# Kernel optimization log

Measured on AMD Instinct MI355X. Metric: run time of the kernel, lower is better.

The kernel has to match this reference:

```python
import jax, jax.numpy as jnp
import numpy as np

EPS = 1e-5        # BatchNorm eps (torch default)
ALPHA = 0.2       # LeakyReLU negative slope


def _gather_nbrs(x, idx):
    # x: (B,N,C), idx: (B,P,S) -> (B,P,S,C)
    B, P, S = idx.shape
    flat = jnp.take_along_axis(x, idx.reshape(B, P * S, 1), axis=1)
    return flat.reshape(B, P, S, x.shape[-1])


def _mlp_layer(x, w, b, g, bt, m, v):
    # 1x1 Conv2d == channel matmul; BN in eval mode with running stats; ReLU.
    h = x @ w.T + b
    h = (h - m) * jax.lax.rsqrt(v + EPS) * g + bt
    return jax.nn.relu(h)


def setup_inputs() -> dict:
    key = jax.random.key(0)
    ks = jax.random.split(key, 8)
    B, N, P, S, C = 16, 4096, 1024, 32, 64
    inp = {
        "xyz": jax.random.normal(ks[0], (B, 3, N), dtype=jnp.float32),
        "points": jax.random.normal(ks[1], (B, C, N), dtype=jnp.float32),
        "fps_idx": jax.random.randint(ks[2], (B, P), 0, N, dtype=jnp.int32),
        "group_idx": jax.random.randint(ks[3], (B, P, S), 0, N, dtype=jnp.int32),
    }
    chans = [(64, 67), (64, 64), (128, 64)]
    for i, (co, ci) in enumerate(chans, start=1):
        kk = jax.random.fold_in(key, 100 + i)
        inp[f"w{i}"] = jax.random.normal(kk, (co, ci), dtype=jnp.float32) * (1.0 / np.sqrt(ci))
        inp[f"b{i}"] = jnp.zeros((co,), jnp.float32)
        inp[f"g{i}"] = jnp.ones((co,), jnp.float32)
        inp[f"beta{i}"] = jnp.zeros((co,), jnp.float32)
        inp[f"m{i}"] = jnp.zeros((co,), jnp.float32)
        inp[f"v{i}"] = jnp.ones((co,), jnp.float32)
    inp["a"] = jax.random.normal(ks[4], (3 + 128, 128), dtype=jnp.float32) * 0.1
    return inp


def reference(xyz, points, fps_idx, group_idx,
              w1, b1, g1, beta1, m1, v1,
              w2, b2, g2, beta2, m2, v2,
              w3, b3, g3, beta3, m3, v3, a):
    xyz_p = jnp.transpose(xyz, (0, 2, 1))      # (B,N,3)
    pts_p = jnp.transpose(points, (0, 2, 1))   # (B,N,C)

    # sample_and_group with precomputed fps / ball-query indices
    new_xyz = jnp.take_along_axis(xyz_p, fps_idx[:, :, None], axis=1)   # (B,P,3)
    fps_feat = jnp.take_along_axis(pts_p, fps_idx[:, :, None], axis=1)  # (B,P,C)
    grouped_xyz = _gather_nbrs(xyz_p, group_idx) - new_xyz[:, :, None, :]  # relative (B,P,S,3)
    grouped_feat = _gather_nbrs(pts_p, group_idx)                           # (B,P,S,C)

    new_points = jnp.concatenate([grouped_xyz, grouped_feat], axis=-1)  # (B,P,S,3+C)
    fps_points = jnp.concatenate([new_xyz, fps_feat], axis=-1)          # (B,P,3+C)

    layers = [(w1, b1, g1, beta1, m1, v1), (w2, b2, g2, beta2, m2, v2), (w3, b3, g3, beta3, m3, v3)]
    for (w, b, g, bt, m, v) in layers:
        new_points = _mlp_layer(new_points, w, b, g, bt, m, v)
        fps_points = _mlp_layer(fps_points, w, b, g, bt, m, v)

    # GraphAttention: delta features -> leaky-relu scores -> softmax over neighbors -> pool
    delta_p = new_xyz[:, :, None, :] - grouped_xyz        # (B,P,S,3)
    delta_h = fps_points[:, :, None, :] - new_points       # (B,P,S,D)
    e = jnp.concatenate([delta_p, delta_h], axis=-1) @ a   # (B,P,S,D)
    e = jnp.where(e > 0, e, ALPHA * e)
    attn = jax.nn.softmax(e, axis=2)                       # softmax over nsample
    pooled = jnp.sum(attn * new_points, axis=2)            # (B,P,D)

    return jnp.transpose(new_xyz, (0, 2, 1)), jnp.transpose(pooled, (0, 2, 1))
```

## Files before the change

kernel.cpp:

```cpp
#include <hip/hip_runtime.h>
#include <hip/hip_bf16.h>

#define Bn 16
#define Nn 4096
#define Pn 1024
#define Sn 32
#define Cn 64
#define EPSn 1e-5f
#define ALPHAn 0.2f
#define LOG2E 1.44269504088896341f

#define W1O 0
#define W2O 4352
#define W3O 8448
#define AO  16640
#define B1O 33536
#define B2O 33600
#define B3O 33664
#define WSF 33792
__device__ __align__(16) float g_W[WSF];

#define F1F 0
#define F2F 24
#define F3F 40
#define F5F 72
#define NFRAG 152
#define WFU (NFRAG * 512)
__device__ __align__(16) unsigned short g_Wf[WFU];

__device__ __align__(16) float g_pts[Bn * Nn * 68];
__device__ __align__(16) float g_fps[Bn * Pn * 132];
__device__ __align__(16) float g_tmp[Bn * Pn * 128];

typedef __attribute__((ext_vector_type(8))) short short8;
typedef __attribute__((ext_vector_type(4))) float f32x4;

__device__ __forceinline__ void split2(float v, unsigned short& hu, unsigned short& lu) {
  __hip_bfloat16 h = __float2bfloat16(v);
  float hv = __bfloat162float(h);
  __hip_bfloat16 l = __float2bfloat16(v - hv);
  hu = *(unsigned short*)&h;
  lu = *(unsigned short*)&l;
}
__device__ __forceinline__ unsigned short bfh(float v) {
  __hip_bfloat16 h = __float2bfloat16(v);
  return *(unsigned short*)&h;
}

#define MFMA_BF16 __builtin_amdgcn_mfma_f32_16x16x32_bf16
#define TERM3(Ci, Ahh, All, Bh, Bl) \
    Ci = MFMA_BF16(Ahh, Bh, Ci, 0, 0, 0); \
    Ci = MFMA_BF16(Ahh, Bl, Ci, 0, 0, 0); \
    Ci = MFMA_BF16(All, Bh, Ci, 0, 0, 0);

#define ST_PK(BUF, ST, ROW, COLE, V) do {                                   \
    float _pp = __shfl_xor((V), 1);                                         \
    unsigned _pk;                                                           \
    asm("v_cvt_pk_bf16_f32 %0, %1, %2" : "=v"(_pk) : "v"(V), "v"(_pp));     \
    if (!(nn & 1)) *(unsigned*)((BUF) + (ROW) * (ST) + (COLE)) = _pk;       \
  } while (0)

__global__ __launch_bounds__(256) void prep_kernel(
    const float* __restrict__ xyz, const float* __restrict__ points,
    const float* __restrict__ w1, const float* __restrict__ b1,
    const float* __restrict__ g1, const float* __restrict__ bt1,
    const float* __restrict__ m1, const float* __restrict__ v1,
    const float* __restrict__ w2, const float* __restrict__ b2,
    const float* __restrict__ g2, const float* __restrict__ bt2,
    const float* __restrict__ m2, const float* __restrict__ v2,
    const float* __restrict__ w3, const float* __restrict__ b3,
    const float* __restrict__ g3, const float* __restrict__ bt3,
    const float* __restrict__ m3, const float* __restrict__ v3,
    const float* __restrict__ a)
{
  if (blockIdx.x < 1024) {
    __shared__ float T[68 * 65];
    const int t = threadIdx.x;
    const int b = blockIdx.x >> 6, n0 = (blockIdx.x & 63) << 6;
    const int nn = t & 63, cgrp = t >> 6;
    #pragma unroll
    for (int k = 0; k < 16; ++k) {
      const int c = cgrp * 16 + k;
      T[c * 65 + nn] = points[(b * Cn + c) * Nn + n0 + nn];
    }
    if (cgrp == 0) {
      #pragma unroll
      for (int d = 0; d < 3; ++d)
        T[(64 + d) * 65 + nn] = xyz[(b * 3 + d) * Nn + n0 + nn];
      T[67 * 65 + nn] = 0.f;
    }
    __syncthreads();
    const int row = t >> 2, part = t & 3;
    float* dst = g_pts + (((long)b << 12) + n0 + row) * 68 + part * 16;
    #pragma unroll
    for (int j = 0; j < 4; ++j) {
      const int o = part * 16 + j * 4;
      float4 v = { T[(o + 0) * 65 + row], T[(o + 1) * 65 + row],
                   T[(o + 2) * 65 + row], T[(o + 3) * 65 + row] };
      *(float4*)(dst + j * 4) = v;
    }
    if (part == 3) {
      float4 v = { T[64 * 65 + row], T[65 * 65 + row],
                   T[66 * 65 + row], T[67 * 65 + row] };
      *(float4*)(dst + 16) = v;
    }
    return;
  }
  const int idx = (blockIdx.x - 1024) * blockDim.x + threadIdx.x;
  if (idx < WSF) {
    float val;
    if (idx < W2O) {
      const int k = idx >> 6, o = idx & 63;
      const float sc = g1[o] * rsqrtf(v1[o] + EPSn);
      val = (k < 64) ? w1[o * 67 + 3 + k] * sc
          : (k < 67) ? w1[o * 67 + (k - 64)] * sc : 0.f;
    } else if (idx < W3O) {
      const int r = idx - W2O, k = r >> 6, o = r & 63;
      val = w2[o * 64 + k] * (g2[o] * rsqrtf(v2[o] + EPSn));
    } else if (idx < AO) {
      const int r = idx - W3O, k = r >> 7, o = r & 127;
      val = w3[o * 64 + k] * (g3[o] * rsqrtf(v3[o] + EPSn));
    } else if (idx < B1O) {
      int r = idx - AO;
      const int half = r / 8448; r -= half * 8448;
      const int k = r >> 6, o = half * 64 + (r & 63);
      val = (k < 128) ? a[(3 + k) * 128 + o]
          : (k < 131) ? a[(k - 128) * 128 + o] : 0.f;
    } else if (idx < B2O) {
      const int o = idx - B1O;
      val = (b1[o] - m1[o]) * (g1[o] * rsqrtf(v1[o] + EPSn)) + bt1[o];
    } else if (idx < B3O) {
      const int o = idx - B2O;
      val = (b2[o] - m2[o]) * (g2[o] * rsqrtf(v2[o] + EPSn)) + bt2[o];
    } else {
      const int o = idx - B3O;
      val = (b3[o] - m3[o]) * (g3[o] * rsqrtf(v3[o] + EPSn)) + bt3[o];
    }
    g_W[idx] = val;
  } else if (idx < WSF + WFU) {
    const int i = idx - WSF;
    const int frag = i >> 9, r = i & 511;
    const int lane = r >> 3, j = r & 7;
    const int quad = lane >> 4, nn = lane & 15;
    int plane, n, k;
    float w;
    if (frag < F2F) {
      const int f = frag;
      plane = f & 1;
      const int c = (f >> 1) & 1, kcch = f >> 2, kc = kcch % 3, ch = kcch / 3;
      n = ch * 32 + c * 16 + nn; k = kc * 32 + quad * 8 + j;
      const float s = g1[n] * rsqrtf(v1[n] + EPSn);
      w = (k < 64) ? w1[n * 67 + 3 + k] * s
        : (k < 67) ? w1[n * 67 + (k - 64)] * s : 0.f;
    } else if (frag < F3F) {
      const int f = frag - F2F;
      plane = f & 1;
      const int c = (f >> 1) & 1, kc = (f >> 2) & 1, ch = f >> 3;
      n = ch * 32 + c * 16 + nn; k = kc * 32 + quad * 8 + j;
      w = w2[n * 64 + k] * (g2[n] * rsqrtf(v2[n] + EPSn));
    } else if (frag < F5F) {
      const int f = frag - F3F;
      plane = f & 1;
      const int c = (f >> 1) & 3, kc = (f >> 3) & 1, ch = f >> 4;
      n = ch * 64 + c * 16 + nn; k = kc * 32 + quad * 8 + j;
      w = w3[n * 64 + k] * (g3[n] * rsqrtf(v3[n] + EPSn));
    } else {
      const int f = frag - F5F;
      plane = f & 1;
      const int c = (f >> 1) & 3, kcch = f >> 3, kc = kcch % 5, ch = kcch / 5;
      n = ch * 64 + c * 16 + nn; k = kc * 32 + quad * 8 + j;
      w = ((k < 128) ? a[(3 + k) * 128 + n]
        : (k < 131) ? a[(k - 128) * 128 + n] : 0.f) * LOG2E;
    }
    unsigned short hu, lu; split2(w, hu, lu);
    g_Wf[i] = plane ? lu : hu;
  }
}

#define XAs 88
#define XHs 152

__global__ __launch_bounds__(256) void fps_kernel(
    const int* __restrict__ fps_idx, float* __restrict__ out)
{
  __shared__ __align__(16) unsigned char LB[15376];
  unsigned short* XAh = (unsigned short*)(LB + 0);
  unsigned short* XAl = (unsigned short*)(LB + 2816);
  unsigned short* XHh = (unsigned short*)(LB + 5632);
  unsigned short* XHl = (unsigned short*)(LB + 10496);
  unsigned short* ZS  = (unsigned short*)(LB + 15360);

  const int t = threadIdx.x, lane = t & 63, w = t >> 6;
  const int quad = lane >> 4, nn = lane & 15;
  const int ch = w >> 1, cl = w & 1;
  const int blk = ((blockIdx.x & 7) << 7) | (blockIdx.x >> 3);
  const int g0 = blk * 16;

  if (t < 4) ((float*)ZS)[t] = 0.f;

  if (t < 128) {
    const int s0 = t >> 3, cg = t & 7;
    const int gp = g0 + s0, b = gp >> 10, p = gp & 1023;
    const int fi = fps_idx[gp];
    const float* frow = g_pts + (((long)b << 12) + fi) * 68;
    const int c0 = cg * 8;
    const float4 va = *(const float4*)(frow + c0);
    const float4 vb = *(const float4*)(frow + c0 + 4);
    short8 hv, lv;
    unsigned short hu, lu;
    split2(va.x, hu, lu); hv[0] = (short)hu; lv[0] = (short)lu;
    split2(va.y, hu, lu); hv[1] = (short)hu; lv[1] = (short)lu;
    split2(va.z, hu, lu); hv[2] = (short)hu; lv[2] = (short)lu;
    split2(va.w, hu, lu); hv[3] = (short)hu; lv[3] = (short)lu;
    split2(vb.x, hu, lu); hv[4] = (short)hu; lv[4] = (short)lu;
    split2(vb.y, hu, lu); hv[5] = (short)hu; lv[5] = (short)lu;
    split2(vb.z, hu, lu); hv[6] = (short)hu; lv[6] = (short)lu;
    split2(vb.w, hu, lu); hv[7] = (short)hu; lv[7] = (short)lu;
    *(short8*)(XAh + s0 * XAs + c0) = hv;
    *(short8*)(XAl + s0 * XAs + c0) = lv;
    if (cg == 0) {
      #pragma unroll
      for (int d = 0; d < 3; ++d) {
        const float v = frow[64 + d];
        unsigned short h2, l2; split2(v, h2, l2);
        XAh[s0 * XAs + 64 + d] = h2; XAl[s0 * XAs + 64 + d] = l2;
        XHh[s0 * XHs + 128 + d] = h2; XHl[s0 * XHs + 131 - 3 + d] = l2;
        XHl[s0 * XHs + 128 + d] = l2;
        out[(b * 3 + d) * Pn + p] = v;
        g_fps[(long)gp * 132 + 128 + d] = v;
      }
    } else if (cg == 1) {
      #pragma unroll
      for (int j = 0; j < 13; ++j) { XAh[s0 * XAs + 67 + j] = 0; XAl[s0 * XAs + 67 + j] = 0; }
    } else if (cg == 2) {
      #pragma unroll
      for (int j = 0; j < 13; ++j) { XHh[s0 * XHs + 131 + j] = 0; XHl[s0 * XHs + 131 + j] = 0; }
    }
  }
  __syncthreads();

  f32x4 C[2];
  const int col1 = w * 16 + nn;

  {
    const float bb = g_W[B1O + col1];
    C[0] = (f32x4){bb, bb, bb, bb};
  }
  #pragma unroll
  for (int kc = 0; kc < 3; ++kc) {
    const int ka = kc * 32 + quad * 8;
    const short8 A0h = (ka < 80) ? *(const short8*)(XAh + nn * XAs + ka) : *(const short8*)ZS;
    const short8 A0l = (ka < 80) ? *(const short8*)(XAl + nn * XAs + ka) : *(const short8*)ZS;
    const unsigned short* pf = g_Wf + (((ch * 3 + kc) * 2 + cl) * 2) * 512 + lane * 8;
    const short8 Bh = *(const short8*)pf, Bl = *(const short8*)(pf + 512);
    TERM3(C[0], A0h, A0l, Bh, Bl);
  }
  #pragma unroll
  for (int r = 0; r < 4; ++r) {
    const float v = fmaxf(C[0][r], 0.f);
    unsigned short hu, lu; split2(v, hu, lu);
    XHh[(quad * 4 + r) * XHs + col1] = hu;
    XHl[(quad * 4 + r) * XHs + col1] = lu;
  }
  __syncthreads();

  {
    const float bb = g_W[B2O + col1];
    C[0] = (f32x4){bb, bb, bb, bb};
  }
  #pragma unroll
  for (int kc = 0; kc < 2; ++kc) {
    const int ka = kc * 32 + quad * 8;
    const short8 A0h = *(const short8*)(XHh + nn * XHs + ka);
    const short8 A0l = *(const short8*)(XHl + nn * XHs + ka);
    const unsigned short* pf = g_Wf + (F2F + ((ch * 2 + kc) * 2 + cl) * 2) * 512 + lane * 8;
    const short8 Bh = *(const short8*)pf, Bl = *(const short8*)(pf + 512);
    TERM3(C[0], A0h, A0l, Bh, Bl);
  }
  __syncthreads();
  #pragma unroll
  for (int r = 0; r < 4; ++r) {
    const float v = fmaxf(C[0][r], 0.f);
    unsigned short hu, lu; split2(v, hu, lu);
    XAh[(quad * 4 + r) * XAs + col1] = hu;
    XAl[(quad * 4 + r) * XAs + col1] = lu;
  }
  __syncthreads();

  {
    const float b0 = g_W[B3O + w * 32 + nn];
    const float b1 = g_W[B3O + w * 32 + 16 + nn];
    C[0] = (f32x4){b0, b0, b0, b0};
    C[1] = (f32x4){b1, b1, b1, b1};
  }
  #pragma unroll
  for (int kc = 0; kc < 2; ++kc) {
    const int ka = kc * 32 + quad * 8;
    const short8 A0h = *(const short8*)(XAh + nn * XAs + ka);
    const short8 A0l = *(const short8*)(XAl + nn * XAs + ka);
    #pragma unroll
    for (int c2 = 0; c2 < 2; ++c2) {
      const unsigned short* pf = g_Wf + (F3F + ((ch * 2 + kc) * 4 + cl * 2 + c2) * 2) * 512 + lane * 8;
      const short8 Bh = *(const short8*)pf, Bl = *(const short8*)(pf + 512);
      TERM3(C[c2], A0h, A0l, Bh, Bl);
    }
  }
  __syncthreads();
  #pragma unroll
  for (int c2 = 0; c2 < 2; ++c2) {
    const int col = w * 32 + c2 * 16 + nn;
    #pragma unroll
    for (int r = 0; r < 4; ++r) {
      const float v = fmaxf(C[c2][r], 0.f);
      unsigned short hu, lu; split2(v, hu, lu);
      XHh[(quad * 4 + r) * XHs + col] = hu;
      XHl[(quad * 4 + r) * XHs + col] = lu;
    }
  }
  __syncthreads();

  C[0] = (f32x4){0.f,0.f,0.f,0.f}; C[1] = C[0];
  #pragma unroll
  for (int kc = 0; kc < 5; ++kc) {
    const int ka = kc * 32 + quad * 8;
    const short8 A0h = (ka < 144) ? *(const short8*)(XHh + nn * XHs + ka) : *(const short8*)ZS;
    const short8 A0l = (ka < 144) ? *(const short8*)(XHl + nn * XHs + ka) : *(const short8*)ZS;
    #pragma unroll
    for (int c2 = 0; c2 < 2; ++c2) {
      const unsigned short* pf = g_Wf + (F5F + ((ch * 5 + kc) * 4 + cl * 2 + c2) * 2) * 512 + lane * 8;
      const short8 Bh = *(const short8*)pf, Bl = *(const short8*)(pf + 512);
      TERM3(C[c2], A0h, A0l, Bh, Bl);
    }
  }
  #pragma unroll
  for (int c2 = 0; c2 < 2; ++c2) {
    const int col = w * 32 + c2 * 16 + nn;
    #pragma unroll
    for (int r = 0; r < 4; ++r)
      g_fps[(long)(g0 + quad * 4 + r) * 132 + col] = C[c2][r];
  }
}

__global__ __launch_bounds__(256) void transpose_out(float* __restrict__ out)
{
  __shared__ float T[64 * 129];
  const int t = threadIdx.x;
  const int b = blockIdx.x >> 4, p0 = (blockIdx.x & 15) << 6;
  const int c = t & 127, ph = t >> 7;
  #pragma unroll
  for (int pp = 0; pp < 32; ++pp) {
    const int pi = ph * 32 + pp;
    T[pi * 129 + c] = g_tmp[(((long)b << 10) + p0 + pi) * 128 + c];
  }
  __syncthreads();
  const int pn = t & 63, cg = t >> 6;
  #pragma unroll
  for (int k = 0; k < 32; ++k) {
    const int cc = cg * 32 + k;
    out[Bn * 3 * Pn + ((b << 7) + cc) * Pn + p0 + pn] = T[pn * 129 + cc];
  }
}

#define OXA 0
#define OXH 5632
#define OZS 15360
#define LDSB 15376

__global__ __launch_bounds__(256, 8) void fused_kernel(
    const int* __restrict__ group_idx)
{
  __shared__ __align__(16) unsigned char LB[LDSB];
  unsigned short* XAh = (unsigned short*)(LB + OXA);
  unsigned short* XHh = (unsigned short*)(LB + OXH);
  unsigned short* ZS  = (unsigned short*)(LB + OZS);

  const int t = threadIdx.x, lane = t & 63, w = t >> 6;
  const int quad = lane >> 4, nn = lane & 15;
  const int ch = w >> 1, cl = w & 1;
  const int g = ((blockIdx.x & 7) << 11) | (blockIdx.x >> 3);
  const int b = g >> 10;

  if (t < 4) ((float*)ZS)[t] = 0.f;

  {
    const int s0 = t >> 3, cg = t & 7;
    const int gi = group_idx[g * Sn + s0];
    const float* prow = g_pts + (((long)b << 12) + gi) * 68;
    const int c0 = cg * 8;
    const float4 va = *(const float4*)(prow + c0);
    const float4 vb = *(const float4*)(prow + c0 + 4);
    unsigned p0, p1, p2, p3;
    asm("v_cvt_pk_bf16_f32 %0, %1, %2" : "=v"(p0) : "v"(va.x), "v"(va.y));
    asm("v_cvt_pk_bf16_f32 %0, %1, %2" : "=v"(p1) : "v"(va.z), "v"(va.w));
    asm("v_cvt_pk_bf16_f32 %0, %1, %2" : "=v"(p2) : "v"(vb.x), "v"(vb.y));
    asm("v_cvt_pk_bf16_f32 %0, %1, %2" : "=v"(p3) : "v"(vb.z), "v"(vb.w));
    uint4 hv = {p0, p1, p2, p3};
    *(uint4*)(XAh + s0 * XAs + c0) = hv;
    if (cg == 0) {
      #pragma unroll
      for (int d = 0; d < 3; ++d) {
        const float r = prow[64 + d] - g_fps[(long)g * 132 + 128 + d];
        const unsigned short hu = bfh(r);
        XAh[s0 * XAs + 64 + d] = hu;
        XHh[s0 * XHs + 128 + d] = hu;
      }
    } else if (cg == 1) {
      #pragma unroll
      for (int j = 0; j < 13; ++j) XAh[s0 * XAs + 67 + j] = 0;
    } else if (cg == 2) {
      #pragma unroll
      for (int j = 0; j < 13; ++j) XHh[s0 * XHs + 131 + j] = 0;
    }
  }
  __syncthreads();

  f32x4 C[4];
  const int col1 = w * 16 + nn;
  const int colE1 = w * 16 + (nn & ~1);

  {
    const float bb = g_W[B1O + col1];
    C[0] = (f32x4){bb, bb, bb, bb};
    C[1] = C[0];
  }
  #pragma unroll
  for (int kc = 0; kc < 3; ++kc) {
    const int ka = kc * 32 + quad * 8;
    const short8 A0 = (ka < 80) ? *(const short8*)(XAh + nn * XAs + ka) : *(const short8*)ZS;
    const short8 A1 = (ka < 80) ? *(const short8*)(XAh + (16 + nn) * XAs + ka) : *(const short8*)ZS;
    const unsigned short* pf = g_Wf + (((ch * 3 + kc) * 2 + cl) * 2) * 512 + lane * 8;
    const short8 Bh = *(const short8*)pf, Bl = *(const short8*)(pf + 512);
    C[0] = MFMA_BF16(A0, Bh, C[0], 0, 0, 0);
    C[0] = MFMA_BF16(A0, Bl, C[0], 0, 0, 0);
    C[1] = MFMA_BF16(A1, Bh, C[1], 0, 0, 0);
    C[1] = MFMA_BF16(A1, Bl, C[1], 0, 0, 0);
  }
  #pragma unroll
  for (int mi = 0; mi < 2; ++mi)
    #pragma unroll
    for (int r = 0; r < 4; ++r) {
      const float v = fmaxf(C[mi][r], 0.f);
      ST_PK(XHh, XHs, mi * 16 + quad * 4 + r, colE1, v);
    }
  __syncthreads();

  {
    const float bb = g_W[B2O + col1];
    C[0] = (f32x4){bb, bb, bb, bb};
    C[1] = C[0];
  }
  #pragma unroll
  for (int kc = 0; kc < 2; ++kc) {
    const int ka = kc * 32 + quad * 8;
    const short8 A0 = *(const short8*)(XHh + nn * XHs + ka);
    const short8 A1 = *(const short8*)(XHh + (16 + nn) * XHs + ka);
    const unsigned short* pf = g_Wf + (F2F + ((ch * 2 + kc) * 2 + cl) * 2) * 512 + lane * 8;
    const short8 Bh = *(const short8*)pf, Bl = *(const short8*)(pf + 512);
    C[0] = MFMA_BF16(A0, Bh, C[0], 0, 0, 0);
    C[0] = MFMA_BF16(A0, Bl, C[0], 0, 0, 0);
    C[1] = MFMA_BF16(A1, Bh, C[1], 0, 0, 0);
    C[1] = MFMA_BF16(A1, Bl, C[1], 0, 0, 0);
  }
  #pragma unroll
  for (int mi = 0; mi < 2; ++mi)
    #pragma unroll
    for (int r = 0; r < 4; ++r) {
      const float v = fmaxf(C[mi][r], 0.f);
      ST_PK(XAh, XAs, mi * 16 + quad * 4 + r, colE1, v);
    }
  __syncthreads();

  {
    const float b0 = g_W[B3O + w * 32 + nn];
    const float b1 = g_W[B3O + w * 32 + 16 + nn];
    C[0] = (f32x4){b0, b0, b0, b0};
    C[1] = (f32x4){b1, b1, b1, b1};
    C[2] = C[0];
    C[3] = C[1];
  }
  #pragma unroll
  for (int kc = 0; kc < 2; ++kc) {
    const int ka = kc * 32 + quad * 8;
    const short8 A0 = *(const short8*)(XAh + nn * XAs + ka);
    const short8 A1 = *(const short8*)(XAh + (16 + nn) * XAs + ka);
    #pragma unroll
    for (int c2 = 0; c2 < 2; ++c2) {
      const unsigned short* pf = g_Wf + (F3F + ((ch * 2 + kc) * 4 + cl * 2 + c2) * 2) * 512 + lane * 8;
      const short8 Bh = *(const short8*)pf, Bl = *(const short8*)(pf + 512);
      C[0 + c2] = MFMA_BF16(A0, Bh, C[0 + c2], 0, 0, 0);
      C[0 + c2] = MFMA_BF16(A0, Bl, C[0 + c2], 0, 0, 0);
      C[2 + c2] = MFMA_BF16(A1, Bh, C[2 + c2], 0, 0, 0);
      C[2 + c2] = MFMA_BF16(A1, Bl, C[2 + c2], 0, 0, 0);
    }
  }
  f32x4 H[4];
  #pragma unroll
  for (int c2 = 0; c2 < 2; ++c2) {
    const int colE = w * 32 + c2 * 16 + (nn & ~1);
    #pragma unroll
    for (int mi = 0; mi < 2; ++mi)
      #pragma unroll
      for (int r = 0; r < 4; ++r) {
        const int idx = mi * 2 + c2;
        const float v = fmaxf(C[idx][r], 0.f);
        H[idx][r] = v;
        ST_PK(XHh, XHs, mi * 16 + quad * 4 + r, colE, v);
      }
  }
  __syncthreads();

  {
    const float e0 = g_fps[(long)g * 132 + w * 32 + nn];
    const float e1 = g_fps[(long)g * 132 + w * 32 + 16 + nn];
    C[0] = (f32x4){-e0, -e0, -e0, -e0};
    C[1] = (f32x4){-e1, -e1, -e1, -e1};
    C[2] = C[0];
    C[3] = C[1];
  }
  #pragma unroll
  for (int kc = 0; kc < 5; ++kc) {
    const int ka = kc * 32 + quad * 8;
    const short8 A0 = (ka < 144) ? *(const short8*)(XHh + nn * XHs + ka) : *(const short8*)ZS;
    const short8 A1 = (ka < 144) ? *(const short8*)(XHh + (16 + nn) * XHs + ka) : *(const short8*)ZS;
    #pragma unroll
    for (int c2 = 0; c2 < 2; ++c2) {
      const unsigned short* pf = g_Wf + (F5F + ((ch * 5 + kc) * 4 + cl * 2 + c2) * 2) * 512 + lane * 8;
      const short8 Bh = *(const short8*)pf, Bl = *(const short8*)(pf + 512);
      C[0 + c2] = MFMA_BF16(A0, Bh, C[0 + c2], 0, 0, 0);
      C[0 + c2] = MFMA_BF16(A0, Bl, C[0 + c2], 0, 0, 0);
      C[2 + c2] = MFMA_BF16(A1, Bh, C[2 + c2], 0, 0, 0);
      C[2 + c2] = MFMA_BF16(A1, Bl, C[2 + c2], 0, 0, 0);
    }
  }

  #pragma unroll
  for (int c2 = 0; c2 < 2; ++c2) {
    float tmin = 3.4e38f;
    #pragma unroll
    for (int mi = 0; mi < 2; ++mi)
      #pragma unroll
      for (int r = 0; r < 4; ++r) {
        const int idx = mi * 2 + c2;
        const float cv = C[idx][r];
        const float tv = fminf(cv, 0.2f * cv);
        C[idx][r] = tv;
        tmin = fminf(tmin, tv);
      }
    tmin = fminf(tmin, __shfl_xor(tmin, 16));
    tmin = fminf(tmin, __shfl_xor(tmin, 32));
    float den = 0.f, pool = 0.f;
    #pragma unroll
    for (int mi = 0; mi < 2; ++mi)
      #pragma unroll
      for (int r = 0; r < 4; ++r) {
        const int idx = mi * 2 + c2;
        const float wgt = __builtin_amdgcn_exp2f(tmin - C[idx][r]);
        den += wgt;
        pool = fmaf(wgt, H[idx][r], pool);
      }
    den  += __shfl_xor(den, 16);  den  += __shfl_xor(den, 32);
    pool += __shfl_xor(pool, 16); pool += __shfl_xor(pool, 32);
    if (quad == 0) {
      const int col = w * 32 + c2 * 16 + nn;
      g_tmp[(long)g * 128 + col] = pool * __builtin_amdgcn_rcpf(den);
    }
  }
}

extern "C" void kernel_launch(void* const* d_in, const int* in_sizes, int n_in,
                              void* d_out, int out_size, void* d_ws, size_t ws_size,
                              hipStream_t stream) {
  const float* xyz       = (const float*)d_in[0];
  const float* points    = (const float*)d_in[1];
  const int*   fps_idx   = (const int*)d_in[2];
  const int*   group_idx = (const int*)d_in[3];

  const int prep_blocks = 1024 + (WSF + WFU + 255) / 256;
  prep_kernel<<<prep_blocks, 256, 0, stream>>>(
      xyz, points,
      (const float*)d_in[4],  (const float*)d_in[5],
      (const float*)d_in[6],  (const float*)d_in[7],
      (const float*)d_in[8],  (const float*)d_in[9],
      (const float*)d_in[10], (const float*)d_in[11],
      (const float*)d_in[12], (const float*)d_in[13],
      (const float*)d_in[14], (const float*)d_in[15],
      (const float*)d_in[16], (const float*)d_in[17],
      (const float*)d_in[18], (const float*)d_in[19],
      (const float*)d_in[20], (const float*)d_in[21],
      (const float*)d_in[22]);

  fps_kernel<<<1024, 256, 0, stream>>>(fps_idx, (float*)d_out);

  fused_kernel<<<Bn * Pn, 256, 0, stream>>>(group_idx);

  transpose_out<<<Bn * 16, 256, 0, stream>>>((float*)d_out);
}
```

Baseline: 250.5 us.

## Process two groups per block, reuse weight fragments, write output directly

```diff
diff --git a/kernel.cpp b/kernel.cpp
--- a/kernel.cpp
+++ b/kernel.cpp
@@ -30,7 +30,6 @@
 
 __device__ __align__(16) float g_pts[Bn * Nn * 68];
 __device__ __align__(16) float g_fps[Bn * Pn * 132];
-__device__ __align__(16) float g_tmp[Bn * Pn * 128];
 
 typedef __attribute__((ext_vector_type(8))) short short8;
 typedef __attribute__((ext_vector_type(4))) float f32x4;
@@ -46,19 +45,16 @@
   __hip_bfloat16 h = __float2bfloat16(v);
   return *(unsigned short*)&h;
 }
+__device__ __forceinline__ float bf2f(unsigned short u) {
+  __hip_bfloat16 h = *(__hip_bfloat16*)&u;
+  return __bfloat162float(h);
+}
 
 #define MFMA_BF16 __builtin_amdgcn_mfma_f32_16x16x32_bf16
 #define TERM3(Ci, Ahh, All, Bh, Bl) \
     Ci = MFMA_BF16(Ahh, Bh, Ci, 0, 0, 0); \
     Ci = MFMA_BF16(Ahh, Bl, Ci, 0, 0, 0); \
     Ci = MFMA_BF16(All, Bh, Ci, 0, 0, 0);
-
-#define ST_PK(BUF, ST, ROW, COLE, V) do {                                   \
-    float _pp = __shfl_xor((V), 1);                                         \
-    unsigned _pk;                                                           \
-    asm("v_cvt_pk_bf16_f32 %0, %1, %2" : "=v"(_pk) : "v"(V), "v"(_pp));     \
-    if (!(nn & 1)) *(unsigned*)((BUF) + (ROW) * (ST) + (COLE)) = _pk;       \
-  } while (0)
 
 __global__ __launch_bounds__(256) void prep_kernel(
     const float* __restrict__ xyz, const float* __restrict__ points,
@@ -224,8 +220,7 @@
         const float v = frow[64 + d];
         unsigned short h2, l2; split2(v, h2, l2);
         XAh[s0 * XAs + 64 + d] = h2; XAl[s0 * XAs + 64 + d] = l2;
-        XHh[s0 * XHs + 128 + d] = h2; XHl[s0 * XHs + 131 - 3 + d] = l2;
-        XHl[s0 * XHs + 128 + d] = l2;
+        XHh[s0 * XHs + 128 + d] = h2; XHl[s0 * XHs + 128 + d] = l2;
         out[(b * 3 + d) * Pn + p] = v;
         g_fps[(long)gp * 132 + 128 + d] = v;
       }
@@ -341,228 +336,256 @@
   }
 }
 
-__global__ __launch_bounds__(256) void transpose_out(float* __restrict__ out)
-{
-  __shared__ float T[64 * 129];
-  const int t = threadIdx.x;
-  const int b = blockIdx.x >> 4, p0 = (blockIdx.x & 15) << 6;
-  const int c = t & 127, ph = t >> 7;
-  #pragma unroll
-  for (int pp = 0; pp < 32; ++pp) {
-    const int pi = ph * 32 + pp;
-    T[pi * 129 + c] = g_tmp[(((long)b << 10) + p0 + pi) * 128 + c];
-  }
-  __syncthreads();
-  const int pn = t & 63, cg = t >> 6;
-  #pragma unroll
-  for (int k = 0; k < 32; ++k) {
-    const int cc = cg * 32 + k;
-    out[Bn * 3 * Pn + ((b << 7) + cc) * Pn + p0 + pn] = T[pn * 129 + cc];
-  }
-}
-
-#define OXA 0
-#define OXH 5632
-#define OZS 15360
-#define LDSB 15376
-
-__global__ __launch_bounds__(256, 8) void fused_kernel(
-    const int* __restrict__ group_idx)
+#define OXA0 0
+#define OXA1 5632
+#define OXH0 11264
+#define OXH1 20992
+#define OFS  30720
+#define OZS  31744
+#define LDSB 31760
+
+__global__ __launch_bounds__(256, 5) void fused_kernel(
+    const int* __restrict__ group_idx, float* __restrict__ out)
 {
   __shared__ __align__(16) unsigned char LB[LDSB];
-  unsigned short* XAh = (unsigned short*)(LB + OXA);
-  unsigned short* XHh = (unsigned short*)(LB + OXH);
-  unsigned short* ZS  = (unsigned short*)(LB + OZS);
+  unsigned short* const XA0 = (unsigned short*)(LB + OXA0);
+  unsigned short* const XA1 = (unsigned short*)(LB + OXA1);
+  unsigned short* const XH0 = (unsigned short*)(LB + OXH0);
+  unsigned short* const XH1 = (unsigned short*)(LB + OXH1);
+  float*          FS = (float*)(LB + OFS);
+  unsigned short* ZS = (unsigned short*)(LB + OZS);
 
   const int t = threadIdx.x, lane = t & 63, w = t >> 6;
   const int quad = lane >> 4, nn = lane & 15;
   const int ch = w >> 1, cl = w & 1;
-  const int g = ((blockIdx.x & 7) << 11) | (blockIdx.x >> 3);
-  const int b = g >> 10;
-
+  const int blk = ((blockIdx.x & 7) << 10) | (blockIdx.x >> 3);
+  const int base = blk * 2;
+  const int b = base >> 10, p0 = base & 1023;
+
+  {
+    const int gi = t >> 7, cc = t & 127;
+    FS[t] = g_fps[(long)(base + gi) * 132 + cc];
+  }
   if (t < 4) ((float*)ZS)[t] = 0.f;
 
   {
     const int s0 = t >> 3, cg = t & 7;
-    const int gi = group_idx[g * Sn + s0];
-    const float* prow = g_pts + (((long)b << 12) + gi) * 68;
     const int c0 = cg * 8;
-    const float4 va = *(const float4*)(prow + c0);
-    const float4 vb = *(const float4*)(prow + c0 + 4);
-    unsigned p0, p1, p2, p3;
-    asm("v_cvt_pk_bf16_f32 %0, %1, %2" : "=v"(p0) : "v"(va.x), "v"(va.y));
-    asm("v_cvt_pk_bf16_f32 %0, %1, %2" : "=v"(p1) : "v"(va.z), "v"(va.w));
-    asm("v_cvt_pk_bf16_f32 %0, %1, %2" : "=v"(p2) : "v"(vb.x), "v"(vb.y));
-    asm("v_cvt_pk_bf16_f32 %0, %1, %2" : "=v"(p3) : "v"(vb.z), "v"(vb.w));
-    uint4 hv = {p0, p1, p2, p3};
-    *(uint4*)(XAh + s0 * XAs + c0) = hv;
-    if (cg == 0) {
-      #pragma unroll
-      for (int d = 0; d < 3; ++d) {
-        const float r = prow[64 + d] - g_fps[(long)g * 132 + 128 + d];
-        const unsigned short hu = bfh(r);
-        XAh[s0 * XAs + 64 + d] = hu;
-        XHh[s0 * XHs + 128 + d] = hu;
+    #pragma unroll
+    for (int gi = 0; gi < 2; ++gi) {
+      unsigned short* XAg = gi ? XA1 : XA0;
+      unsigned short* XHg = gi ? XH1 : XH0;
+      const int gidx = group_idx[(base + gi) * Sn + s0];
+      const float* prow = g_pts + (((long)b << 12) + gidx) * 68;
+      const float4 va = *(const float4*)(prow + c0);
+      const float4 vb = *(const float4*)(prow + c0 + 4);
+      unsigned q0, q1, q2, q3;
+      asm("v_cvt_pk_bf16_f32 %0, %1, %2" : "=v"(q0) : "v"(va.x), "v"(va.y));
+      asm("v_cvt_pk_bf16_f32 %0, %1, %2" : "=v"(q1) : "v"(va.z), "v"(va.w));
+      asm("v_cvt_pk_bf16_f32 %0, %1, %2" : "=v"(q2) : "v"(vb.x), "v"(vb.y));
+      asm("v_cvt_pk_bf16_f32 %0, %1, %2" : "=v"(q3) : "v"(vb.z), "v"(vb.w));
+      uint4 hv = {q0, q1, q2, q3};
+      *(uint4*)(XAg + s0 * XAs + c0) = hv;
+      if (cg == 0) {
+        #pragma unroll
+        for (int d = 0; d < 3; ++d) {
+          const float r = prow[64 + d] - g_fps[(long)(base + gi) * 132 + 128 + d];
+          const unsigned short hu = bfh(r);
+          XAg[s0 * XAs + 64 + d] = hu;
+          XHg[s0 * XHs + 128 + d] = hu;
+        }
+      } else if (cg == 1) {
+        #pragma unroll
+        for (int j = 0; j < 13; ++j) XAg[s0 * XAs + 67 + j] = 0;
+      } else if (cg == 2) {
+        #pragma unroll
+        for (int j = 0; j < 13; ++j) XHg[s0 * XHs + 131 + j] = 0;
       }
-    } else if (cg == 1) {
-      #pragma unroll
-      for (int j = 0; j < 13; ++j) XAh[s0 * XAs + 67 + j] = 0;
-    } else if (cg == 2) {
-      #pragma unroll
-      for (int j = 0; j < 13; ++j) XHh[s0 * XHs + 131 + j] = 0;
-    }
-  }
-  __syncthreads();
-
-  f32x4 C[4];
+    }
+  }
+  __syncthreads();
+
   const int col1 = w * 16 + nn;
-  const int colE1 = w * 16 + (nn & ~1);
-
-  {
+
+  {
+    f32x4 C00, C01, C10, C11;
     const float bb = g_W[B1O + col1];
-    C[0] = (f32x4){bb, bb, bb, bb};
-    C[1] = C[0];
-  }
-  #pragma unroll
-  for (int kc = 0; kc < 3; ++kc) {
-    const int ka = kc * 32 + quad * 8;
-    const short8 A0 = (ka < 80) ? *(const short8*)(XAh + nn * XAs + ka) : *(const short8*)ZS;
-    const short8 A1 = (ka < 80) ? *(const short8*)(XAh + (16 + nn) * XAs + ka) : *(const short8*)ZS;
-    const unsigned short* pf = g_Wf + (((ch * 3 + kc) * 2 + cl) * 2) * 512 + lane * 8;
-    const short8 Bh = *(const short8*)pf, Bl = *(const short8*)(pf + 512);
-    C[0] = MFMA_BF16(A0, Bh, C[0], 0, 0, 0);
-    C[0] = MFMA_BF16(A0, Bl, C[0], 0, 0, 0);
-    C[1] = MFMA_BF16(A1, Bh, C[1], 0, 0, 0);
-    C[1] = MFMA_BF16(A1, Bl, C[1], 0, 0, 0);
-  }
-  #pragma unroll
-  for (int mi = 0; mi < 2; ++mi)
+    C00 = (f32x4){bb, bb, bb, bb};
+    C01 = C00; C10 = C00; C11 = C00;
+    #pragma unroll
+    for (int kc = 0; kc < 3; ++kc) {
+      const int ka = kc * 32 + quad * 8;
+      const unsigned short* pf = g_Wf + (((ch * 3 + kc) * 2 + cl) * 2) * 512 + lane * 8;
+      const short8 Bh = *(const short8*)pf, Bl = *(const short8*)(pf + 512);
+      const short8 A00 = (ka < 80) ? *(const short8*)(XA0 + nn * XAs + ka) : *(const short8*)ZS;
+      const short8 A01 = (ka < 80) ? *(const short8*)(XA0 + (16 + nn) * XAs + ka) : *(const short8*)ZS;
+      const short8 A10 = (ka < 80) ? *(const short8*)(XA1 + nn * XAs + ka) : *(const short8*)ZS;
+      const short8 A11 = (ka < 80) ? *(const short8*)(XA1 + (16 + nn) * XAs + ka) : *(const short8*)ZS;
+      C00 = MFMA_BF16(A00, Bh, C00, 0, 0, 0);
+      C00 = MFMA_BF16(A00, Bl, C00, 0, 0, 0);
+      C01 = MFMA_BF16(A01, Bh, C01, 0, 0, 0);
+      C01 = MFMA_BF16(A01, Bl, C01, 0, 0, 0);
+      C10 = MFMA_BF16(A10, Bh, C10, 0, 0, 0);
+      C10 = MFMA_BF16(A10, Bl, C10, 0, 0, 0);
+      C11 = MFMA_BF16(A11, Bh, C11, 0, 0, 0);
+      C11 = MFMA_BF16(A11, Bl, C11, 0, 0, 0);
+    }
     #pragma unroll
     for (int r = 0; r < 4; ++r) {
-      const float v = fmaxf(C[mi][r], 0.f);
-      ST_PK(XHh, XHs, mi * 16 + quad * 4 + r, colE1, v);
-    }
-  __syncthreads();
-
-  {
+      XH0[(quad * 4 + r) * XHs + col1]      = bfh(fmaxf(C00[r], 0.f));
+      XH0[(16 + quad * 4 + r) * XHs + col1] = bfh(fmaxf(C01[r], 0.f));
+      XH1[(quad * 4 + r) * XHs + col1]      = bfh(fmaxf(C10[r], 0.f));
+      XH1[(16 + quad * 4 + r) * XHs + col1] = bfh(fmaxf(C11[r], 0.f));
+    }
+  }
+  __syncthreads();
+
+  {
+    f32x4 C00, C01, C10, C11;
     const float bb = g_W[B2O + col1];
-    C[0] = (f32x4){bb, bb, bb, bb};
-    C[1] = C[0];
-  }
-  #pragma unroll
-  for (int kc = 0; kc < 2; ++kc) {
-    const int ka = kc * 32 + quad * 8;
-    const short8 A0 = *(const short8*)(XHh + nn * XHs + ka);
-    const short8 A1 = *(const short8*)(XHh + (16 + nn) * XHs + ka);
-    const unsigned short* pf = g_Wf + (F2F + ((ch * 2 + kc) * 2 + cl) * 2) * 512 + lane * 8;
-    const short8 Bh = *(const short8*)pf, Bl = *(const short8*)(pf + 512);
-    C[0] = MFMA_BF16(A0, Bh, C[0], 0, 0, 0);
-    C[0] = MFMA_BF16(A0, Bl, C[0], 0, 0, 0);
-    C[1] = MFMA_BF16(A1, Bh, C[1], 0, 0, 0);
-    C[1] = MFMA_BF16(A1, Bl, C[1], 0, 0, 0);
-  }
-  #pragma unroll
-  for (int mi = 0; mi < 2; ++mi)
+    C00 = (f32x4){bb, bb, bb, bb};
+    C01 = C00; C10 = C00; C11 = C00;
+    #pragma unroll
+    for (int kc = 0; kc < 2; ++kc) {
+      const int ka = kc * 32 + quad * 8;
+      const unsigned short* pf = g_Wf + (F2F + ((ch * 2 + kc) * 2 + cl) * 2) * 512 + lane * 8;
+      const short8 Bh = *(const short8*)pf, Bl = *(const short8*)(pf + 512);
+      const short8 A00 = *(const short8*)(XH0 + nn * XHs + ka);
+      const short8 A01 = *(const short8*)(XH0 + (16 + nn) * XHs + ka);
+      const short8 A10 = *(const short8*)(XH1 + nn * XHs + ka);
+      const short8 A11 = *(const short8*)(XH1 + (16 + nn) * XHs + ka);
+      C00 = MFMA_BF16(A00, Bh, C00, 0, 0, 0);
+      C00 = MFMA_BF16(A00, Bl, C00, 0, 0, 0);
+      C01 = MFMA_BF16(A01, Bh, C01, 0, 0, 0);
+      C01 = MFMA_BF16(A01, Bl, C01, 0, 0, 0);
+      C10 = MFMA_BF16(A10, Bh, C10, 0, 0, 0);
+      C10 = MFMA_BF16(A10, Bl, C10, 0, 0, 0);
+      C11 = MFMA_BF16(A11, Bh, C11, 0, 0, 0);
+      C11 = MFMA_BF16(A11, Bl, C11, 0, 0, 0);
+    }
     #pragma unroll
     for (int r = 0; r < 4; ++r) {
-      const float v = fmaxf(C[mi][r], 0.f);
-      ST_PK(XAh, XAs, mi * 16 + quad * 4 + r, colE1, v);
-    }
-  __syncthreads();
-
-  {
+      XA0[(quad * 4 + r) * XAs + col1]      = bfh(fmaxf(C00[r], 0.f));
+      XA0[(16 + quad * 4 + r) * XAs + col1] = bfh(fmaxf(C01[r], 0.f));
+      XA1[(quad * 4 + r) * XAs + col1]      = bfh(fmaxf(C10[r], 0.f));
+      XA1[(16 + quad * 4 + r) * XAs + col1] = bfh(fmaxf(C11[r], 0.f));
+    }
+  }
+  __syncthreads();
+
+  {
+    f32x4 C0[4], C1[4];
     const float b0 = g_W[B3O + w * 32 + nn];
     const float b1 = g_W[B3O + w * 32 + 16 + nn];
-    C[0] = (f32x4){b0, b0, b0, b0};
-    C[1] = (f32x4){b1, b1, b1, b1};
-    C[2] = C[0];
-    C[3] = C[1];
-  }
-  #pragma unroll
-  for (int kc = 0; kc < 2; ++kc) {
-    const int ka = kc * 32 + quad * 8;
-    const short8 A0 = *(const short8*)(XAh + nn * XAs + ka);
-    const short8 A1 = *(const short8*)(XAh + (16 + nn) * XAs + ka);
+    C0[0] = (f32x4){b0, b0, b0, b0};
+    C0[1] = (f32x4){b1, b1, b1, b1};
+    C0[2] = C0[0]; C0[3] = C0[1];
+    C1[0] = C0[0]; C1[1] = C0[1]; C1[2] = C0[0]; C1[3] = C0[1];
+    #pragma unroll
+    for (int kc = 0; kc < 2; ++kc) {
+      const int ka = kc * 32 + quad * 8;
+      const short8 A00 = *(const short8*)(XA0 + nn * XAs + ka);
+      const short8 A01 = *(const short8*)(XA0 + (16 + nn) * XAs + ka);
+      const short8 A10 = *(const short8*)(XA1 + nn * XAs + ka);
+      const short8 A11 = *(const short8*)(XA1 + (16 + nn) * XAs + ka);
+      #pragma unroll
+      for (int c2 = 0; c2 < 2; ++c2) {
+        const unsigned short* pf = g_Wf + (F3F + ((ch * 2 + kc) * 4 + cl * 2 + c2) * 2) * 512 + lane * 8;
+        const short8 Bh = *(const short8*)pf, Bl = *(const short8*)(pf + 512);
+        C0[0 + c2] = MFMA_BF16(A00, Bh, C0[0 + c2], 0, 0, 0);
+        C0[0 + c2] = MFMA_BF16(A00, Bl, C0[0 + c2], 0, 0, 0);
+        C0[2 + c2] = MFMA_BF16(A01, Bh, C0[2 + c2], 0, 0, 0);
+        C0[2 + c2] = MFMA_BF16(A01, Bl, C0[2 + c2], 0, 0, 0);
+        C1[0 + c2] = MFMA_BF16(A10, Bh, C1[0 + c2], 0, 0, 0);
+        C1[0 + c2] = MFMA_BF16(A10, Bl, C1[0 + c2], 0, 0, 0);
+        C1[2 + c2] = MFMA_BF16(A11, Bh, C1[2 + c2], 0, 0, 0);
+        C1[2 + c2] = MFMA_BF16(A11, Bl, C1[2 + c2], 0, 0, 0);
+      }
+    }
     #pragma unroll
     for (int c2 = 0; c2 < 2; ++c2) {
-      const unsigned short* pf = g_Wf + (F3F + ((ch * 2 + kc) * 4 + cl * 2 + c2) * 2) * 512 + lane * 8;
-      const short8 Bh = *(const short8*)pf, Bl = *(const short8*)(pf + 512);
-      C[0 + c2] = MFMA_BF16(A0, Bh, C[0 + c2], 0, 0, 0);
-      C[0 + c2] = MFMA_BF16(A0, Bl, C[0 + c2], 0, 0, 0);
-      C[2 + c2] = MFMA_BF16(A1, Bh, C[2 + c2], 0, 0, 0);
-      C[2 + c2] = MFMA_BF16(A1, Bl, C[2 + c2], 0, 0, 0);
-    }
-  }
-  f32x4 H[4];
-  #pragma unroll
-  for (int c2 = 0; c2 < 2; ++c2) {
-    const int colE = w * 32 + c2 * 16 + (nn & ~1);
-    #pragma unroll
-    for (int mi = 0; mi < 2; ++mi)
+      const int col = w * 32 + c2 * 16 + nn;
       #pragma unroll
       for (int r = 0; r < 4; ++r) {
-        const int idx = mi * 2 + c2;
-        const float v = fmaxf(C[idx][r], 0.f);
-        H[idx][r] = v;
-        ST_PK(XHh, XHs, mi * 16 + quad * 4 + r, colE, v);
+        XH0[(quad * 4 + r) * XHs + col]      = bfh(fmaxf(C0[0 + c2][r], 0.f));
+        XH0[(16 + quad * 4 + r) * XHs + col] = bfh(fmaxf(C0[2 + c2][r], 0.f));
+        XH1[(quad * 4 + r) * XHs + col]      = bfh(fmaxf(C1[0 + c2][r], 0.f));
+        XH1[(16 + quad * 4 + r) * XHs + col] = bfh(fmaxf(C1[2 + c2][r], 0.f));
       }
-  }
-  __syncthreads();
-
-  {
-    const float e0 = g_fps[(long)g * 132 + w * 32 + nn];
-    const float e1 = g_fps[(long)g * 132 + w * 32 + 16 + nn];
-    C[0] = (f32x4){-e0, -e0, -e0, -e0};
-    C[1] = (f32x4){-e1, -e1, -e1, -e1};
-    C[2] = C[0];
-    C[3] = C[1];
+    }
+  }
+  __syncthreads();
+
+  f32x4 C0[4], C1[4];
+  {
+    const float e00 = FS[w * 32 + nn];
+    const float e01 = FS[w * 32 + 16 + nn];
+    const float e10 = FS[128 + w * 32 + nn];
+    const float e11 = FS[128 + w * 32 + 16 + nn];
+    C0[0] = (f32x4){-e00, -e00, -e00, -e00};
+    C0[1] = (f32x4){-e01, -e01, -e01, -e01};
+    C0[2] = C0[0]; C0[3] = C0[1];
+    C1[0] = (f32x4){-e10, -e10, -e10, -e10};
+    C1[1] = (f32x4){-e11, -e11, -e11, -e11};
+    C1[2] = C1[0]; C1[3] = C1[1];
   }
   #pragma unroll
   for (int kc = 0; kc < 5; ++kc) {
     const int ka = kc * 32 + quad * 8;
-    const short8 A0 = (ka < 144) ? *(const short8*)(XHh + nn * XHs + ka) : *(const short8*)ZS;
-    const short8 A1 = (ka < 144) ? *(const short8*)(XHh + (16 + nn) * XHs + ka) : *(const short8*)ZS;
+    const short8 A00 = (ka < 144) ? *(const short8*)(XH0 + nn * XHs + ka) : *(const short8*)ZS;
+    const short8 A01 = (ka < 144) ? *(const short8*)(XH0 + (16 + nn) * XHs + ka) : *(const short8*)ZS;
+    const short8 A10 = (ka < 144) ? *(const short8*)(XH1 + nn * XHs + ka) : *(const short8*)ZS;
+    const short8 A11 = (ka < 144) ? *(const short8*)(XH1 + (16 + nn) * XHs + ka) : *(const short8*)ZS;
     #pragma unroll
     for (int c2 = 0; c2 < 2; ++c2) {
       const unsigned short* pf = g_Wf + (F5F + ((ch * 5 + kc) * 4 + cl * 2 + c2) * 2) * 512 + lane * 8;
       const short8 Bh = *(const short8*)pf, Bl = *(const short8*)(pf + 512);
-      C[0 + c2] = MFMA_BF16(A0, Bh, C[0 + c2], 0, 0, 0);
-      C[0 + c2] = MFMA_BF16(A0, Bl, C[0 + c2], 0, 0, 0);
-      C[2 + c2] = MFMA_BF16(A1, Bh, C[2 + c2], 0, 0, 0);
-      C[2 + c2] = MFMA_BF16(A1, Bl, C[2 + c2], 0, 0, 0);
-    }
-  }
-
-  #pragma unroll
-  for (int c2 = 0; c2 < 2; ++c2) {
-    float tmin = 3.4e38f;
-    #pragma unroll
-    for (int mi = 0; mi < 2; ++mi)
-      #pragma unroll
-      for (int r = 0; r < 4; ++r) {
-        const int idx = mi * 2 + c2;
-        const float cv = C[idx][r];
-        const float tv = fminf(cv, 0.2f * cv);
-        C[idx][r] = tv;
-        tmin = fminf(tmin, tv);
-      }
-    tmin = fminf(tmin, __shfl_xor(tmin, 16));
-    tmin = fminf(tmin, __shfl_xor(tmin, 32));
-    float den = 0.f, pool = 0.f;
-    #pragma unroll
-    for (int mi = 0; mi < 2; ++mi)
-      #pragma unroll
-      for (int r = 0; r < 4; ++r) {
-        const int idx = mi * 2 + c2;
-        const float wgt = __builtin_amdgcn_exp2f(tmin - C[idx][r]);
-        den += wgt;
-        pool = fmaf(wgt, H[idx][r], pool);
-      }
-    den  += __shfl_xor(den, 16);  den  += __shfl_xor(den, 32);
-    pool += __shfl_xor(pool, 16); pool += __shfl_xor(pool, 32);
-    if (quad == 0) {
+      C0[0 + c2] = MFMA_BF16(A00, Bh, C0[0 + c2], 0, 0, 0);
+      C0[0 + c2] = MFMA_BF16(A00, Bl, C0[0 + c2], 0, 0, 0);
+      C0[2 + c2] = MFMA_BF16(A01, Bh, C0[2 + c2], 0, 0, 0);
+      C0[2 + c2] = MFMA_BF16(A01, Bl, C0[2 + c2], 0, 0, 0);
+      C1[0 + c2] = MFMA_BF16(A10, Bh, C1[0 + c2], 0, 0, 0);
+      C1[0 + c2] = MFMA_BF16(A10, Bl, C1[0 + c2], 0, 0, 0);
+      C1[2 + c2] = MFMA_BF16(A11, Bh, C1[2 + c2], 0, 0, 0);
+      C1[2 + c2] = MFMA_BF16(A11, Bl, C1[2 + c2], 0, 0, 0);
+    }
+  }
+
+  #pragma unroll
+  for (int gi = 0; gi < 2; ++gi) {
+    unsigned short* XHg = gi ? XH1 : XH0;
+    #pragma unroll
+    for (int c2 = 0; c2 < 2; ++c2) {
       const int col = w * 32 + c2 * 16 + nn;
-      g_tmp[(long)g * 128 + col] = pool * __builtin_amdgcn_rcpf(den);
+      f32x4* Cg = gi ? C1 : C0;
+      float tmin = 3.4e38f;
+      #pragma unroll
+      for (int mi = 0; mi < 2; ++mi)
+        #pragma unroll
+        for (int r = 0; r < 4; ++r) {
+          const int idx = mi * 2 + c2;
+          const float cv = Cg[idx][r];
+          const float tv = fminf(cv, 0.2f * cv);
+          Cg[idx][r] = tv;
+          tmin = fminf(tmin, tv);
+        }
+      tmin = fminf(tmin, __shfl_xor(tmin, 16));
+      tmin = fminf(tmin, __shfl_xor(tmin, 32));
+      float den = 0.f, pool = 0.f;
+      #pragma unroll
+      for (int mi = 0; mi < 2; ++mi)
+        #pragma unroll
+        for (int r = 0; r < 4; ++r) {
+          const int idx = mi * 2 + c2;
+          const float wgt = __builtin_amdgcn_exp2f(tmin - Cg[idx][r]);
+          den += wgt;
+          pool = fmaf(wgt, bf2f(XHg[(mi * 16 + quad * 4 + r) * XHs + col]), pool);
+        }
+      den  += __shfl_xor(den, 16);  den  += __shfl_xor(den, 32);
+      pool += __shfl_xor(pool, 16); pool += __shfl_xor(pool, 32);
+      if (quad == 0)
+        out[Bn * 3 * Pn + ((b << 7) + col) * Pn + p0 + gi] =
+            pool * __builtin_amdgcn_rcpf(den);
     }
   }
 }
@@ -591,7 +614,5 @@
 
   fps_kernel<<<1024, 256, 0, stream>>>(fps_idx, (float*)d_out);
 
-  fused_kernel<<<Bn * Pn, 256, 0, stream>>>(group_idx);
-
-  transpose_out<<<Bn * 16, 256, 0, stream>>>((float*)d_out);
+  fused_kernel<<<Bn * Pn / 2, 256, 0, stream>>>(group_idx, (float*)d_out);
 }
```

Result: faster. 221.5 us (-11.6%).
